# Performance work log

Measured on AMD Instinct MI355X. Metric: run time of the kernel, lower is better.

Reference implementation:

```python
import jax, jax.numpy as jnp
import numpy as np

C, N, H, OUT, NIN, NSRC, NB = 16, 8192, 181, 3, 2, 32, 8
OMEGA, SCALE = 30.0, 10.0


def _c(a):
    # view trailing dim-2 float array as complex
    return jax.lax.complex(a[..., 0], a[..., 1])


def setup_inputs() -> dict:
    key = jax.random.key(0)
    ks = jax.random.split(key, 20)
    d = {}
    d["inp"] = jax.random.normal(ks[0], (NSRC, N, NIN), jnp.float32)
    d["indices"] = jax.random.randint(ks[1], (C,), 0, NSRC)
    d["model_idx"] = jax.random.randint(ks[2], (C,), 0, C)
    d["bias_idx"] = jax.random.randint(ks[3], (C,), 0, NB)
    # first layer (real weights, in=2)
    d["W0a"] = 0.05 * jax.random.normal(ks[4], (C, NIN, H), jnp.float32)
    d["b0a"] = 0.01 * jax.random.normal(ks[5], (NB, H), jnp.float32)
    d["W0b"] = 0.05 * jax.random.normal(ks[6], (C, NIN, H), jnp.float32)
    d["b0b"] = 0.01 * jax.random.normal(ks[7], (NB, H), jnp.float32)
    # hidden complex layers stored as float[..., 2] (real, imag)
    k = 8
    for name in ["W1a", "b1a", "W1b", "b1b", "W2a", "b2a", "W2b", "b2b"]:
        if name.startswith("W"):
            d[name] = 0.01 * jax.random.normal(ks[k], (C, H, H, 2), jnp.float32)
        else:
            d[name] = 0.01 * jax.random.normal(ks[k], (NB, H, 2), jnp.float32)
        k += 1
    d["Wf"] = 0.05 * jax.random.normal(ks[16], (C, H, OUT, 2), jnp.float32)
    d["bf"] = 0.01 * jax.random.normal(ks[17], (NB, OUT, 2), jnp.float32)
    return d


def _forward(inp, indices, model_idx, bias_idx, W0a, b0a, W0b, b0b,
             W1a, b1a, W1b, b1b, W2a, b2a, W2b, b2b, Wf, bf):
    x = inp[None, indices]  # [1, C, N, in]
    # first Gabor2D layer: real adaptive linear, complex exp activation
    la = jnp.einsum('bcni,cio->bcno', x, W0a[model_idx]) + b0a[bias_idx][None, :, None, :]
    lb = jnp.einsum('bcni,cio->bcno', x, W0b[model_idx]) + b0b[bias_idx][None, :, None, :]
    # exp(1j*omega*la - |scale*la|^2 - |scale*lb|^2), la/lb real here
    x = jnp.exp(jax.lax.complex(-(SCALE * SCALE) * (la * la + lb * lb), OMEGA * la))
    # hidden Gabor2D layers: complex adaptive linear, fused Gabor chain
    for Wa, ba, Wb, bb in ((W1a, b1a, W1b, b1b), (W2a, b2a, W2b, b2b)):
        la = jnp.einsum('bcni,cio->bcno', x, _c(Wa)[model_idx]) + _c(ba)[bias_idx][None, :, None, :]
        lb = jnp.einsum('bcni,cio->bcno', x, _c(Wb)[model_idx]) + _c(bb)[bias_idx][None, :, None, :]
        # arg = 1j*omega*la - scale^2*(|la|^2 + |lb|^2)
        mag = (SCALE * SCALE) * (la.real ** 2 + la.imag ** 2 + lb.real ** 2 + lb.imag ** 2)
        x = jnp.exp(jax.lax.complex(-OMEGA * la.imag - mag, OMEGA * la.real))
    # outermost complex linear; module returns .real for complex output
    out = jnp.einsum('bcni,cio->bcno', x, _c(Wf)[model_idx]) + _c(bf)[bias_idx][None, :, None, :]
    return out.real


def reference(inp, indices, model_idx, bias_idx, W0a, b0a, W0b, b0b,
              W1a, b1a, W1b, b1b, W2a, b2a, W2b, b2b, Wf, bf):
    return _forward(inp, indices, model_idx, bias_idx, W0a, b0a, W0b, b0b,
                    W1a, b1a, W1b, b1b, W2a, b2a, W2b, b2b, Wf, bf)
```

## Files before the change

kernel.cpp:

```cpp
#include <hip/hip_runtime.h>

typedef _Float16 f16;
typedef _Float16 f16x2 __attribute__((ext_vector_type(2)));
typedef _Float16 f16x8 __attribute__((ext_vector_type(8)));
typedef float f32x4 __attribute__((ext_vector_type(4)));

namespace {

constexpr int kC = 16, kN = 8192, kH = 181, kOut = 3;
constexpr int kMB = 64;
constexpr int kKpad = 384;
constexpr int kNT = 48;
constexpr int kKS = 12;
constexpr int kRowB = 784;
constexpr float kOmega = 30.f, kS2 = 100.f;

constexpr size_t kWLayerStride = (size_t)kNT * kKS * 64 * 8;
constexpr size_t kWfOff = kWLayerStride * kC * 2;
constexpr size_t kWfStride = (size_t)kKS * 64 * 8;
constexpr size_t kW0Off = kWfOff + (size_t)kC * kWfStride;
constexpr size_t kW0Stride = (size_t)kNT * 64 * 8;

__device__ __forceinline__ int xadr(int row, int colb) { return row * kRowB + colb; }

__global__ __launch_bounds__(768) void prep_hidden(
    const int* __restrict__ model_idx,
    const float* __restrict__ W1a, const float* __restrict__ W1b,
    const float* __restrict__ W2a, const float* __restrict__ W2b,
    f16* __restrict__ ws)
{
  __shared__ float s[kH][2][4][2];
  const int bid = blockIdx.x;
  const int c  = bid / (2 * kNT);
  const int L  = (bid / kNT) % 2;
  const int nt = bid % kNT;
  const int m  = model_idx[c];
  const float* Wa = (L == 0 ? W1a : W2a) + (size_t)m * kH * kH * 2;
  const float* Wb = (L == 0 ? W1b : W2b) + (size_t)m * kH * kH * 2;
  const int t = threadIdx.x;
  if (t < 2 * kH) {
    const int i = t >> 1, br = t & 1;
    const float* src = (br ? Wb : Wa) + ((size_t)i * kH + nt * 4) * 2;
#pragma unroll
    for (int e = 0; e < 8; ++e) {
      const int osub = e >> 1, reim = e & 1;
      s[i][br][osub][reim] = (nt * 4 + osub < kH) ? src[osub * 2 + reim] : 0.f;
    }
  }
  __syncthreads();
  const int ks = t >> 6, lane = t & 63;
  const int kg = lane >> 4, l15 = lane & 15;
  const int osub = l15 >> 2, comp = l15 & 3, br = comp >> 1;
  const int o = nt * 4 + osub;
  f16x8 v;
#pragma unroll
  for (int j = 0; j < 8; ++j) {
    const int k = ks * 32 + kg * 8 + j;
    float f = 0.f;
    if (k < 2 * kH && o < kH) {
      const int i = k >> 1, kodd = k & 1;
      const int reim = kodd ? (1 - (comp & 1)) : (comp & 1);
      f = s[i][br][osub][reim];
      if (kodd && !(comp & 1)) f = -f;
    }
    v[j] = (f16)f;
  }
  *(f16x8*)&ws[(((size_t)(c * 2 + L) * kNT + nt) * kKS + ks) * 512 + lane * 8] = v;
}

__global__ __launch_bounds__(768) void prep_final(
    const int* __restrict__ model_idx, const float* __restrict__ Wf,
    f16* __restrict__ ws)
{
  const int c = blockIdx.x;
  const int m = model_idx[c];
  const int t = threadIdx.x;
  const int ks = t >> 6, lane = t & 63;
  const int kg = lane >> 4, col = lane & 15;
  f16x8 v;
#pragma unroll
  for (int j = 0; j < 8; ++j) {
    const int k = ks * 32 + kg * 8 + j;
    float f = 0.f;
    if (k < 2 * kH && col < kOut) {
      const int i = k >> 1;
      const float* p = &Wf[(((size_t)m * kH + i) * kOut + col) * 2];
      f = (k & 1) ? -p[1] : p[0];
    }
    v[j] = (f16)f;
  }
  *(f16x8*)&ws[kWfOff + ((size_t)c * kKS + ks) * 512 + lane * 8] = v;
}

__global__ __launch_bounds__(256) void prep_l0(
    const int* __restrict__ model_idx,
    const float* __restrict__ W0a, const float* __restrict__ W0b,
    f16* __restrict__ ws)
{
  const int c = blockIdx.x;
  const int m = model_idx[c];
#pragma unroll 1
  for (int it = 0; it < 12; ++it) {
    const int slot = it * 256 + threadIdx.x;
    const int nt = slot >> 6, lane = slot & 63;
    const int kg = lane >> 4, l15 = lane & 15;
    const int osub = l15 >> 2, comp = l15 & 3;
    const int o = nt * 4 + osub;
    f16x8 v = {};
    if (kg == 0 && o < kH && (comp & 1) == 0) {
#pragma unroll
      for (int k = 0; k < 2; ++k) {
        const float f = (comp == 0) ? W0a[(m * 2 + k) * kH + o]
                                    : W0b[(m * 2 + k) * kH + o];
        v[k] = (f16)f;
      }
    }
    *(f16x8*)&ws[kW0Off + (size_t)c * kW0Stride + (size_t)slot * 8] = v;
  }
}

__device__ __forceinline__ void hidden_gemm(
    char* __restrict__ X, const f16x8* __restrict__ wl,
    const float* __restrict__ ba, const float* __restrict__ bb,
    int w, int lane)
{
  const int kg = lane >> 4, l15 = lane & 15;
  f16x8 B[4][kKS];
#pragma unroll
  for (int pt = 0; pt < 4; ++pt)
#pragma unroll
    for (int ks = 0; ks < kKS; ++ks)
      B[pt][ks] = *(const f16x8*)(X + xadr(l15 + 16 * pt, ks * 64 + kg * 16));
  __syncthreads();

#pragma unroll 1
  for (int mi = 0; mi < 12; ++mi) {
    const int nt = w * 12 + mi;
    const int q = nt * 4 + kg;
    const f16x8* ap = wl + (size_t)nt * (kKS * 64) + lane;
    f32x4 acc[4] = {};
    __builtin_amdgcn_s_setprio(1);
#pragma unroll
    for (int ks = 0; ks < kKS; ++ks) {
      const f16x8 a = ap[ks * 64];
      acc[0] = __builtin_amdgcn_mfma_f32_16x16x32_f16(a, B[0][ks], acc[0], 0, 0, 0);
      acc[1] = __builtin_amdgcn_mfma_f32_16x16x32_f16(a, B[1][ks], acc[1], 0, 0, 0);
      acc[2] = __builtin_amdgcn_mfma_f32_16x16x32_f16(a, B[2][ks], acc[2], 0, 0, 0);
      acc[3] = __builtin_amdgcn_mfma_f32_16x16x32_f16(a, B[3][ks], acc[3], 0, 0, 0);
    }
    __builtin_amdgcn_s_setprio(0);
    float br_ = 0.f, bi_ = 0.f, cr_ = 0.f, ci_ = 0.f;
    if (q < kH) {
      const float2 bav = *(const float2*)&ba[q * 2];
      const float2 bbv = *(const float2*)&bb[q * 2];
      br_ = bav.x; bi_ = bav.y; cr_ = bbv.x; ci_ = bbv.y;
    }
#pragma unroll
    for (int pt = 0; pt < 4; ++pt) {
      const float v0 = acc[pt][0] + br_, v1 = acc[pt][1] + bi_;
      const float v2 = acc[pt][2] + cr_, v3 = acc[pt][3] + ci_;
      const float mag = kS2 * (v0 * v0 + v1 * v1 + v2 * v2 + v3 * v3);
      const float amp = __expf(fmaf(-kOmega, v1, -mag));
      const float ph  = kOmega * v0;
      f16x2 pv = {(f16)(amp * __cosf(ph)), (f16)(amp * __sinf(ph))};
      *(f16x2*)(X + xadr(l15 + 16 * pt, q * 4)) = pv;
    }
  }
}

__global__ __launch_bounds__(256, 2)
void wire_main(
    const float* __restrict__ inp, const int* __restrict__ indices,
    const int* __restrict__ model_idx, const int* __restrict__ bias_idx,
    const float* __restrict__ b0a, const float* __restrict__ b0b,
    const float* __restrict__ b1a, const float* __restrict__ b1b,
    const float* __restrict__ b2a, const float* __restrict__ b2b,
    const float* __restrict__ bf, const f16* __restrict__ wsW,
    float* __restrict__ out)
{
  __shared__ __align__(16) char X[kMB * kRowB];
  const int d = blockIdx.x;
  const int lg = (d & 7) * 256 + (d >> 3);
  const int c = lg >> 7;
  const int n0 = (lg & 127) * kMB;
  const int src = indices[c], m = model_idx[c], bix = bias_idx[c];
  const int tid = threadIdx.x, w = tid >> 6, lane = tid & 63;
  const int kg = lane >> 4, l15 = lane & 15;

  {
    f16x8 Bx[4];
#pragma unroll
    for (int pt = 0; pt < 4; ++pt) {
      const int row = l15 + 16 * pt;
      const float2 xv = *(const float2*)&inp[((size_t)src * kN + n0 + row) * 2];
      f16x8 b = {};
      if (kg == 0) { b[0] = (f16)xv.x; b[1] = (f16)xv.y; }
      Bx[pt] = b;
    }
    const f16x8* w0p = (const f16x8*)(wsW + kW0Off + (size_t)c * kW0Stride);
    const float* b0av = b0a + (size_t)bix * kH;
    const float* b0bv = b0b + (size_t)bix * kH;
#pragma unroll 1
    for (int mi = 0; mi < 12; ++mi) {
      const int nt = w * 12 + mi;
      const int q = nt * 4 + kg;
      const f16x8 a = w0p[nt * 64 + lane];
      f32x4 acc[4] = {};
      __builtin_amdgcn_s_setprio(1);
      acc[0] = __builtin_amdgcn_mfma_f32_16x16x32_f16(a, Bx[0], acc[0], 0, 0, 0);
      acc[1] = __builtin_amdgcn_mfma_f32_16x16x32_f16(a, Bx[1], acc[1], 0, 0, 0);
      acc[2] = __builtin_amdgcn_mfma_f32_16x16x32_f16(a, Bx[2], acc[2], 0, 0, 0);
      acc[3] = __builtin_amdgcn_mfma_f32_16x16x32_f16(a, Bx[3], acc[3], 0, 0, 0);
      __builtin_amdgcn_s_setprio(0);
      float br_ = 0.f, cr_ = 0.f;
      if (q < kH) { br_ = b0av[q]; cr_ = b0bv[q]; }
#pragma unroll
      for (int pt = 0; pt < 4; ++pt) {
        const float v0 = acc[pt][0] + br_;
        const float v2 = acc[pt][2] + cr_;
        const float mag = kS2 * (v0 * v0 + v2 * v2);
        const float amp = __expf(-mag);
        const float ph  = kOmega * v0;
        f16x2 pv = {(f16)(amp * __cosf(ph)), (f16)(amp * __sinf(ph))};
        *(f16x2*)(&X[0] + xadr(l15 + 16 * pt, q * 4)) = pv;
      }
    }
  }
  __syncthreads();
  hidden_gemm(X, (const f16x8*)(wsW + (size_t)(c * 2 + 0) * kWLayerStride),
              b1a + (size_t)bix * kH * 2, b1b + (size_t)bix * kH * 2, w, lane);
  __syncthreads();
  hidden_gemm(X, (const f16x8*)(wsW + (size_t)(c * 2 + 1) * kWLayerStride),
              b2a + (size_t)bix * kH * 2, b2b + (size_t)bix * kH * 2, w, lane);
  __syncthreads();
  {
    const f16x8* wf = (const f16x8*)(wsW + kWfOff + (size_t)c * kWfStride);
    f32x4 facc = {0.f, 0.f, 0.f, 0.f};
#pragma unroll
    for (int ks = 0; ks < kKS; ++ks) {
      f16x8 a = *(const f16x8*)(&X[0] + xadr(l15 + 16 * w, ks * 64 + kg * 16));
      f16x8 b = wf[(size_t)ks * 64 + lane];
      facc = __builtin_amdgcn_mfma_f32_16x16x32_f16(a, b, facc, 0, 0, 0);
    }
    if (l15 < kOut) {
      const float bfr = bf[(bix * kOut + l15) * 2];
#pragma unroll
      for (int j = 0; j < 4; ++j) {
        const int row = w * 16 + kg * 4 + j;
        out[((size_t)c * kN + n0 + row) * kOut + l15] = facc[j] + bfr;
      }
    }
  }
}

}

extern "C" void kernel_launch(void* const* d_in, const int* in_sizes, int n_in,
                              void* d_out, int out_size, void* d_ws, size_t ws_size,
                              hipStream_t stream) {
  const float* inp       = (const float*)d_in[0];
  const int*   indices   = (const int*)  d_in[1];
  const int*   model_idx = (const int*)  d_in[2];
  const int*   bias_idx  = (const int*)  d_in[3];
  const float* W0a = (const float*)d_in[4];
  const float* b0a = (const float*)d_in[5];
  const float* W0b = (const float*)d_in[6];
  const float* b0b = (const float*)d_in[7];
  const float* W1a = (const float*)d_in[8];
  const float* b1a = (const float*)d_in[9];
  const float* W1b = (const float*)d_in[10];
  const float* b1b = (const float*)d_in[11];
  const float* W2a = (const float*)d_in[12];
  const float* b2a = (const float*)d_in[13];
  const float* W2b = (const float*)d_in[14];
  const float* b2b = (const float*)d_in[15];
  const float* Wf  = (const float*)d_in[16];
  const float* bff = (const float*)d_in[17];
  f16*   ws  = (f16*)d_ws;
  float* out = (float*)d_out;

  prep_hidden<<<dim3(kC * 2 * kNT), dim3(768), 0, stream>>>(model_idx, W1a, W1b, W2a, W2b, ws);
  prep_final<<<dim3(kC), dim3(768), 0, stream>>>(model_idx, Wf, ws);
  prep_l0<<<dim3(kC), dim3(256), 0, stream>>>(model_idx, W0a, W0b, ws);
  wire_main<<<dim3(kC * (kN / kMB)), dim3(256), 0, stream>>>(
      inp, indices, model_idx, bias_idx, b0a, b0b,
      b1a, b1b, b2a, b2b, bff, ws, out);
}
```

Before: 219.9 us.

## Make each wave own 16 rows through all layers, removing block barriers

Each wave now keeps a private 16-row slab of the activation tile and computes all 48 output tiles per layer for those rows, so every __syncthreads between layers disappears. Biases are folded into the accumulator's initial value, and launch bounds are raised to allow 3 blocks per CU. In exchange, each weight fragment is reused over 16 rows instead of 64, so weight loads per block rise about fourfold. Each output tile is also a single dependent chain of 12 MFMAs, with less independent work available to hide latency.

```diff
diff --git a/kernel.cpp b/kernel.cpp
--- a/kernel.cpp
+++ b/kernel.cpp
@@ -119,56 +119,45 @@
   }
 }
 
-__device__ __forceinline__ void hidden_gemm(
-    char* __restrict__ X, const f16x8* __restrict__ wl,
+__device__ __forceinline__ void hidden_layer_wave(
+    char* __restrict__ slab, const f16x8* __restrict__ wl,
     const float* __restrict__ ba, const float* __restrict__ bb,
-    int w, int lane)
+    int lane)
 {
   const int kg = lane >> 4, l15 = lane & 15;
-  f16x8 B[4][kKS];
-#pragma unroll
-  for (int pt = 0; pt < 4; ++pt)
-#pragma unroll
-    for (int ks = 0; ks < kKS; ++ks)
-      B[pt][ks] = *(const f16x8*)(X + xadr(l15 + 16 * pt, ks * 64 + kg * 16));
-  __syncthreads();
+  f16x8 B[kKS];
+#pragma unroll
+  for (int ks = 0; ks < kKS; ++ks)
+    B[ks] = *(const f16x8*)(slab + xadr(l15, ks * 64 + kg * 16));
 
 #pragma unroll 1
-  for (int mi = 0; mi < 12; ++mi) {
-    const int nt = w * 12 + mi;
+  for (int nt = 0; nt < kNT; ++nt) {
     const int q = nt * 4 + kg;
     const f16x8* ap = wl + (size_t)nt * (kKS * 64) + lane;
-    f32x4 acc[4] = {};
-    __builtin_amdgcn_s_setprio(1);
-#pragma unroll
-    for (int ks = 0; ks < kKS; ++ks) {
-      const f16x8 a = ap[ks * 64];
-      acc[0] = __builtin_amdgcn_mfma_f32_16x16x32_f16(a, B[0][ks], acc[0], 0, 0, 0);
-      acc[1] = __builtin_amdgcn_mfma_f32_16x16x32_f16(a, B[1][ks], acc[1], 0, 0, 0);
-      acc[2] = __builtin_amdgcn_mfma_f32_16x16x32_f16(a, B[2][ks], acc[2], 0, 0, 0);
-      acc[3] = __builtin_amdgcn_mfma_f32_16x16x32_f16(a, B[3][ks], acc[3], 0, 0, 0);
-    }
-    __builtin_amdgcn_s_setprio(0);
-    float br_ = 0.f, bi_ = 0.f, cr_ = 0.f, ci_ = 0.f;
+    f16x8 a[kKS];
+#pragma unroll
+    for (int ks = 0; ks < kKS; ++ks) a[ks] = ap[ks * 64];
+    f32x4 acc = {};
     if (q < kH) {
       const float2 bav = *(const float2*)&ba[q * 2];
       const float2 bbv = *(const float2*)&bb[q * 2];
-      br_ = bav.x; bi_ = bav.y; cr_ = bbv.x; ci_ = bbv.y;
-    }
-#pragma unroll
-    for (int pt = 0; pt < 4; ++pt) {
-      const float v0 = acc[pt][0] + br_, v1 = acc[pt][1] + bi_;
-      const float v2 = acc[pt][2] + cr_, v3 = acc[pt][3] + ci_;
-      const float mag = kS2 * (v0 * v0 + v1 * v1 + v2 * v2 + v3 * v3);
-      const float amp = __expf(fmaf(-kOmega, v1, -mag));
-      const float ph  = kOmega * v0;
-      f16x2 pv = {(f16)(amp * __cosf(ph)), (f16)(amp * __sinf(ph))};
-      *(f16x2*)(X + xadr(l15 + 16 * pt, q * 4)) = pv;
-    }
-  }
-}
-
-__global__ __launch_bounds__(256, 2)
+      acc = f32x4{bav.x, bav.y, bbv.x, bbv.y};
+    }
+    __builtin_amdgcn_s_setprio(1);
+#pragma unroll
+    for (int ks = 0; ks < kKS; ++ks)
+      acc = __builtin_amdgcn_mfma_f32_16x16x32_f16(a[ks], B[ks], acc, 0, 0, 0);
+    __builtin_amdgcn_s_setprio(0);
+    const float v0 = acc[0], v1 = acc[1], v2 = acc[2], v3 = acc[3];
+    const float mag = kS2 * (v0 * v0 + v1 * v1 + v2 * v2 + v3 * v3);
+    const float amp = __expf(fmaf(-kOmega, v1, -mag));
+    const float ph  = kOmega * v0;
+    f16x2 pv = {(f16)(amp * __cosf(ph)), (f16)(amp * __sinf(ph))};
+    *(f16x2*)(slab + xadr(l15, q * 4)) = pv;
+  }
+}
+
+__global__ __launch_bounds__(256, 3)
 void wire_main(
     const float* __restrict__ inp, const int* __restrict__ indices,
     const int* __restrict__ model_idx, const int* __restrict__ bias_idx,
@@ -186,59 +175,41 @@
   const int src = indices[c], m = model_idx[c], bix = bias_idx[c];
   const int tid = threadIdx.x, w = tid >> 6, lane = tid & 63;
   const int kg = lane >> 4, l15 = lane & 15;
+  char* slab = &X[(16 * w) * kRowB];
 
   {
-    f16x8 Bx[4];
-#pragma unroll
-    for (int pt = 0; pt < 4; ++pt) {
-      const int row = l15 + 16 * pt;
-      const float2 xv = *(const float2*)&inp[((size_t)src * kN + n0 + row) * 2];
-      f16x8 b = {};
-      if (kg == 0) { b[0] = (f16)xv.x; b[1] = (f16)xv.y; }
-      Bx[pt] = b;
-    }
+    const int row = 16 * w + l15;
+    const float2 xv = *(const float2*)&inp[((size_t)src * kN + n0 + row) * 2];
+    f16x8 bx = {};
+    if (kg == 0) { bx[0] = (f16)xv.x; bx[1] = (f16)xv.y; }
     const f16x8* w0p = (const f16x8*)(wsW + kW0Off + (size_t)c * kW0Stride);
     const float* b0av = b0a + (size_t)bix * kH;
     const float* b0bv = b0b + (size_t)bix * kH;
 #pragma unroll 1
-    for (int mi = 0; mi < 12; ++mi) {
-      const int nt = w * 12 + mi;
+    for (int nt = 0; nt < kNT; ++nt) {
       const int q = nt * 4 + kg;
       const f16x8 a = w0p[nt * 64 + lane];
-      f32x4 acc[4] = {};
-      __builtin_amdgcn_s_setprio(1);
-      acc[0] = __builtin_amdgcn_mfma_f32_16x16x32_f16(a, Bx[0], acc[0], 0, 0, 0);
-      acc[1] = __builtin_amdgcn_mfma_f32_16x16x32_f16(a, Bx[1], acc[1], 0, 0, 0);
-      acc[2] = __builtin_amdgcn_mfma_f32_16x16x32_f16(a, Bx[2], acc[2], 0, 0, 0);
-      acc[3] = __builtin_amdgcn_mfma_f32_16x16x32_f16(a, Bx[3], acc[3], 0, 0, 0);
-      __builtin_amdgcn_s_setprio(0);
-      float br_ = 0.f, cr_ = 0.f;
-      if (q < kH) { br_ = b0av[q]; cr_ = b0bv[q]; }
-#pragma unroll
-      for (int pt = 0; pt < 4; ++pt) {
-        const float v0 = acc[pt][0] + br_;
-        const float v2 = acc[pt][2] + cr_;
-        const float mag = kS2 * (v0 * v0 + v2 * v2);
-        const float amp = __expf(-mag);
-        const float ph  = kOmega * v0;
-        f16x2 pv = {(f16)(amp * __cosf(ph)), (f16)(amp * __sinf(ph))};
-        *(f16x2*)(&X[0] + xadr(l15 + 16 * pt, q * 4)) = pv;
-      }
-    }
-  }
-  __syncthreads();
-  hidden_gemm(X, (const f16x8*)(wsW + (size_t)(c * 2 + 0) * kWLayerStride),
-              b1a + (size_t)bix * kH * 2, b1b + (size_t)bix * kH * 2, w, lane);
-  __syncthreads();
-  hidden_gemm(X, (const f16x8*)(wsW + (size_t)(c * 2 + 1) * kWLayerStride),
-              b2a + (size_t)bix * kH * 2, b2b + (size_t)bix * kH * 2, w, lane);
-  __syncthreads();
+      f32x4 acc = {};
+      if (q < kH) acc = f32x4{b0av[q], 0.f, b0bv[q], 0.f};
+      acc = __builtin_amdgcn_mfma_f32_16x16x32_f16(a, bx, acc, 0, 0, 0);
+      const float v0 = acc[0], v2 = acc[2];
+      const float mag = kS2 * (v0 * v0 + v2 * v2);
+      const float amp = __expf(-mag);
+      const float ph  = kOmega * v0;
+      f16x2 pv = {(f16)(amp * __cosf(ph)), (f16)(amp * __sinf(ph))};
+      *(f16x2*)(slab + xadr(l15, q * 4)) = pv;
+    }
+  }
+  hidden_layer_wave(slab, (const f16x8*)(wsW + (size_t)(c * 2 + 0) * kWLayerStride),
+                    b1a + (size_t)bix * kH * 2, b1b + (size_t)bix * kH * 2, lane);
+  hidden_layer_wave(slab, (const f16x8*)(wsW + (size_t)(c * 2 + 1) * kWLayerStride),
+                    b2a + (size_t)bix * kH * 2, b2b + (size_t)bix * kH * 2, lane);
   {
     const f16x8* wf = (const f16x8*)(wsW + kWfOff + (size_t)c * kWfStride);
     f32x4 facc = {0.f, 0.f, 0.f, 0.f};
 #pragma unroll
     for (int ks = 0; ks < kKS; ++ks) {
-      f16x8 a = *(const f16x8*)(&X[0] + xadr(l15 + 16 * w, ks * 64 + kg * 16));
+      f16x8 a = *(const f16x8*)(slab + xadr(l15, ks * 64 + kg * 16));
       f16x8 b = wf[(size_t)ks * 64 + lane];
       facc = __builtin_amdgcn_mfma_f32_16x16x32_f16(a, b, facc, 0, 0, 0);
     }
```

Result: slower. 361.0 us (+64.2%).

## Software-pipeline weight fragment loads across iterations and prepack padded hidden biases

Applied to the files above, without the earlier changes.

Restructures the hidden-layer MFMA loop so weight fragments are loaded two k-steps ahead through a rotating three-window register buffer. The prefetch carries over into the next output tile, and sched_barriers pin the load/MFMA interleave. Hidden-layer biases are also prepacked by the prep kernel into a zero-padded float4-per-output layout in the workspace, which removes the branchy two-pointer bias loads. The goal is to hide global-load latency behind MFMAs. The cost is more live registers, and the final prefetch reads past the layer into the adjacent workspace region.

```diff
diff --git a/kernel.cpp b/kernel.cpp
--- a/kernel.cpp
+++ b/kernel.cpp
@@ -20,13 +20,16 @@
 constexpr size_t kWfStride = (size_t)kKS * 64 * 8;
 constexpr size_t kW0Off = kWfOff + (size_t)kC * kWfStride;
 constexpr size_t kW0Stride = (size_t)kNT * 64 * 8;
+constexpr size_t kBiasOff = kW0Off + (size_t)kC * kW0Stride;
 
 __device__ __forceinline__ int xadr(int row, int colb) { return row * kRowB + colb; }
 
 __global__ __launch_bounds__(768) void prep_hidden(
-    const int* __restrict__ model_idx,
+    const int* __restrict__ model_idx, const int* __restrict__ bias_idx,
     const float* __restrict__ W1a, const float* __restrict__ W1b,
     const float* __restrict__ W2a, const float* __restrict__ W2b,
+    const float* __restrict__ b1a, const float* __restrict__ b1b,
+    const float* __restrict__ b2a, const float* __restrict__ b2b,
     f16* __restrict__ ws)
 {
   __shared__ float s[kH][2][4][2];
@@ -47,6 +50,17 @@
       s[i][br][osub][reim] = (nt * 4 + osub < kH) ? src[osub * 2 + reim] : 0.f;
     }
   }
+  if (t < 16) {
+    const int bix = bias_idx[c];
+    const float* pa = (L == 0 ? b1a : b2a) + (size_t)bix * kH * 2;
+    const float* pb = (L == 0 ? b1b : b2b) + (size_t)bix * kH * 2;
+    const int osub = t >> 2, j = t & 3;
+    const int q = nt * 4 + osub;
+    float v = 0.f;
+    if (q < kH) v = (j < 2) ? pa[q * 2 + j] : pb[q * 2 + (j - 2)];
+    float* fb = (float*)(ws + kBiasOff);
+    fb[((size_t)(c * 2 + L) * 192 + nt * 4) * 4 + t] = v;
+  }
   __syncthreads();
   const int ks = t >> 6, lane = t & 63;
   const int kg = lane >> 4, l15 = lane & 15;
@@ -119,9 +133,23 @@
   }
 }
 
+#define ISSUE2(WIN, J0) { WIN[0] = ap[(J0) * 64]; WIN[1] = ap[(J0 + 1) * 64]; }
+#define SLOT2(WIN, KSB)                                                        \
+  __builtin_amdgcn_sched_barrier(0);                                           \
+  __builtin_amdgcn_s_setprio(1);                                               \
+  _Pragma("unroll")                                                            \
+  for (int k2 = 0; k2 < 2; ++k2) {                                             \
+    acc[0] = __builtin_amdgcn_mfma_f32_16x16x32_f16(WIN[k2], B[0][(KSB) + k2], acc[0], 0, 0, 0); \
+    acc[1] = __builtin_amdgcn_mfma_f32_16x16x32_f16(WIN[k2], B[1][(KSB) + k2], acc[1], 0, 0, 0); \
+    acc[2] = __builtin_amdgcn_mfma_f32_16x16x32_f16(WIN[k2], B[2][(KSB) + k2], acc[2], 0, 0, 0); \
+    acc[3] = __builtin_amdgcn_mfma_f32_16x16x32_f16(WIN[k2], B[3][(KSB) + k2], acc[3], 0, 0, 0); \
+  }                                                                            \
+  __builtin_amdgcn_s_setprio(0);                                               \
+  __builtin_amdgcn_sched_barrier(0);
+
 __device__ __forceinline__ void hidden_gemm(
     char* __restrict__ X, const f16x8* __restrict__ wl,
-    const float* __restrict__ ba, const float* __restrict__ bb,
+    const float* __restrict__ bp,
     int w, int lane)
 {
   const int kg = lane >> 4, l15 = lane & 15;
@@ -132,33 +160,31 @@
     for (int ks = 0; ks < kKS; ++ks)
       B[pt][ks] = *(const f16x8*)(X + xadr(l15 + 16 * pt, ks * 64 + kg * 16));
   __syncthreads();
+
+  f16x8 A0[2], A1[2], A2[2];
+  {
+    const f16x8* ap = wl + (size_t)(w * 12) * (kKS * 64) + lane;
+    ISSUE2(A0, 0)
+    ISSUE2(A1, 2)
+  }
 
 #pragma unroll 1
   for (int mi = 0; mi < 12; ++mi) {
     const int nt = w * 12 + mi;
     const int q = nt * 4 + kg;
     const f16x8* ap = wl + (size_t)nt * (kKS * 64) + lane;
+    const f32x4 bv = *(const f32x4*)(bp + (size_t)q * 4);
     f32x4 acc[4] = {};
-    __builtin_amdgcn_s_setprio(1);
-#pragma unroll
-    for (int ks = 0; ks < kKS; ++ks) {
-      const f16x8 a = ap[ks * 64];
-      acc[0] = __builtin_amdgcn_mfma_f32_16x16x32_f16(a, B[0][ks], acc[0], 0, 0, 0);
-      acc[1] = __builtin_amdgcn_mfma_f32_16x16x32_f16(a, B[1][ks], acc[1], 0, 0, 0);
-      acc[2] = __builtin_amdgcn_mfma_f32_16x16x32_f16(a, B[2][ks], acc[2], 0, 0, 0);
-      acc[3] = __builtin_amdgcn_mfma_f32_16x16x32_f16(a, B[3][ks], acc[3], 0, 0, 0);
-    }
-    __builtin_amdgcn_s_setprio(0);
-    float br_ = 0.f, bi_ = 0.f, cr_ = 0.f, ci_ = 0.f;
-    if (q < kH) {
-      const float2 bav = *(const float2*)&ba[q * 2];
-      const float2 bbv = *(const float2*)&bb[q * 2];
-      br_ = bav.x; bi_ = bav.y; cr_ = bbv.x; ci_ = bbv.y;
-    }
+    ISSUE2(A2, 4)   SLOT2(A0, 0)
+    ISSUE2(A0, 6)   SLOT2(A1, 2)
+    ISSUE2(A1, 8)   SLOT2(A2, 4)
+    ISSUE2(A2, 10)  SLOT2(A0, 6)
+    ISSUE2(A0, 12)  SLOT2(A1, 8)
+    ISSUE2(A1, 14)  SLOT2(A2, 10)
 #pragma unroll
     for (int pt = 0; pt < 4; ++pt) {
-      const float v0 = acc[pt][0] + br_, v1 = acc[pt][1] + bi_;
-      const float v2 = acc[pt][2] + cr_, v3 = acc[pt][3] + ci_;
+      const float v0 = acc[pt][0] + bv[0], v1 = acc[pt][1] + bv[1];
+      const float v2 = acc[pt][2] + bv[2], v3 = acc[pt][3] + bv[3];
       const float mag = kS2 * (v0 * v0 + v1 * v1 + v2 * v2 + v3 * v3);
       const float amp = __expf(fmaf(-kOmega, v1, -mag));
       const float ph  = kOmega * v0;
@@ -173,8 +199,6 @@
     const float* __restrict__ inp, const int* __restrict__ indices,
     const int* __restrict__ model_idx, const int* __restrict__ bias_idx,
     const float* __restrict__ b0a, const float* __restrict__ b0b,
-    const float* __restrict__ b1a, const float* __restrict__ b1b,
-    const float* __restrict__ b2a, const float* __restrict__ b2b,
     const float* __restrict__ bf, const f16* __restrict__ wsW,
     float* __restrict__ out)
 {
@@ -227,11 +251,12 @@
     }
   }
   __syncthreads();
+  const float* biasB = (const float*)(wsW + kBiasOff);
   hidden_gemm(X, (const f16x8*)(wsW + (size_t)(c * 2 + 0) * kWLayerStride),
-              b1a + (size_t)bix * kH * 2, b1b + (size_t)bix * kH * 2, w, lane);
+              biasB + (size_t)(c * 2 + 0) * 192 * 4, w, lane);
   __syncthreads();
   hidden_gemm(X, (const f16x8*)(wsW + (size_t)(c * 2 + 1) * kWLayerStride),
-              b2a + (size_t)bix * kH * 2, b2b + (size_t)bix * kH * 2, w, lane);
+              biasB + (size_t)(c * 2 + 1) * 192 * 4, w, lane);
   __syncthreads();
   {
     const f16x8* wf = (const f16x8*)(wsW + kWfOff + (size_t)c * kWfStride);
@@ -279,10 +304,11 @@
   f16*   ws  = (f16*)d_ws;
   float* out = (float*)d_out;
 
-  prep_hidden<<<dim3(kC * 2 * kNT), dim3(768), 0, stream>>>(model_idx, W1a, W1b, W2a, W2b, ws);
+  prep_hidden<<<dim3(kC * 2 * kNT), dim3(768), 0, stream>>>(
+      model_idx, bias_idx, W1a, W1b, W2a, W2b, b1a, b1b, b2a, b2b, ws);
   prep_final<<<dim3(kC), dim3(768), 0, stream>>>(model_idx, Wf, ws);
   prep_l0<<<dim3(kC), dim3(256), 0, stream>>>(model_idx, W0a, W0b, ws);
   wire_main<<<dim3(kC * (kN / kMB)), dim3(256), 0, stream>>>(
       inp, indices, model_idx, bias_idx, b0a, b0b,
-      b1a, b1b, b2a, b2b, bff, ws, out);
-}
+      bff, ws, out);
+}
```

New measurement: 187.7 us. 14.7% less time.
